# Kernel tuning notes

Hardware: AMD Instinct MI355X
Metric: run time of the kernel (lower is better)

Reference implementation:

```python
import jax, jax.numpy as jnp
import numpy as np

B, T, D = 2, 2048, 1024
H = 16
DK = D // H


def setup_inputs() -> dict:
    key = jax.random.key(0)
    ks = jax.random.split(key, 5)
    s = 1.0 / np.sqrt(D)
    return {
        "x": jax.random.normal(ks[0], (B, T, D), dtype=jnp.float32),
        "Wq": jax.random.normal(ks[1], (D, D), dtype=jnp.float32) * s,
        "bq": jnp.zeros((D,), dtype=jnp.float32),
        "Wk": jax.random.normal(ks[2], (D, D), dtype=jnp.float32) * s,
        "bk": jnp.zeros((D,), dtype=jnp.float32),
        "Wv": jax.random.normal(ks[3], (D, D), dtype=jnp.float32) * s,
        "bv": jnp.zeros((D,), dtype=jnp.float32),
        "Wo": jax.random.normal(ks[4], (D, D), dtype=jnp.float32) * s,
        "bo": jnp.zeros((D,), dtype=jnp.float32),
    }


def reference(x, Wq, bq, Wk, bk, Wv, bv, Wo, bo):
    # projections (torch Linear: x @ W.T + b; here W is stored as (in, out))
    Q = x @ Wq + bq  # (B,T,D)
    K = x @ Wk + bk
    V = x @ Wv + bv
    # split heads -> (B,H,T,dk)
    Q = Q.reshape(B, T, H, DK).transpose(0, 2, 1, 3)
    K = K.reshape(B, T, H, DK).transpose(0, 2, 1, 3)
    V = V.reshape(B, T, H, DK).transpose(0, 2, 1, 3)
    scale = 1.0 / jnp.sqrt(jnp.asarray(DK, dtype=x.dtype))
    scores = jnp.einsum("bhqd,bhkd->bhqk", Q, K) * scale  # (B,H,T,T)
    causal = jnp.tril(jnp.ones((T, T), dtype=bool))
    scores = jnp.where(causal, scores, -jnp.inf)
    weights = jax.nn.softmax(scores, axis=-1)
    # dropout is identity in eval mode
    context = jnp.einsum("bhqk,bhkd->bhqd", weights, V)
    context = context.transpose(0, 2, 1, 3).reshape(B, T, D)
    return context @ Wo + bo
```

## Files before the change

### kernel.cpp

```cpp
#include <hip/hip_runtime.h>
#include <hip/hip_bf16.h>

constexpr int Bc = 2;
constexpr int Tc = 2048;
constexpr int Mc = Bc * Tc;
constexpr float CfQ = 0.18033688011112042f;

typedef __attribute__((ext_vector_type(8))) __bf16 bf16x8;
typedef __attribute__((ext_vector_type(4))) __bf16 bf16x4;
typedef __attribute__((ext_vector_type(4))) float floatx4;

__device__ __forceinline__ void gl_lds16(const void* g, void* l) {
    __builtin_amdgcn_global_load_lds(
        (const __attribute__((address_space(1))) void*)g,
        (__attribute__((address_space(3))) void*)l, 16, 0, 0);
}

__global__ __launch_bounds__(256) void prep_all(const float* __restrict__ x,
                                                const float* __restrict__ Wq,
                                                const float* __restrict__ Wk,
                                                const float* __restrict__ Wv,
                                                const float* __restrict__ Wo,
                                                __bf16* __restrict__ xb,
                                                __bf16* __restrict__ Wqkv,
                                                __bf16* __restrict__ Wot) {
    const int z = blockIdx.z;
    const int tid = threadIdx.x;
    if (z >= 4) {
        const int lb = blockIdx.y * 16 + blockIdx.x;
        const size_t base = ((size_t)(z - 4) * 256 + lb) * 4096;
#pragma unroll
        for (int it = 0; it < 4; ++it) {
            const size_t i = base + (size_t)(it * 256 + tid) * 4;
            const float4 v = *(const float4*)(x + i);
            bf16x4 r;
            r[0] = (__bf16)v.x; r[1] = (__bf16)v.y;
            r[2] = (__bf16)v.z; r[3] = (__bf16)v.w;
            *(bf16x4*)(xb + i) = r;
        }
        return;
    }
    __shared__ float t[64][65];
    const float* W = (z == 0) ? Wq : (z == 1) ? Wk : (z == 2) ? Wv : Wo;
    __bf16* Wt = (z < 3) ? Wqkv + (size_t)z * 1024 * 1024 : Wot;
    const int k0 = blockIdx.y * 64, n0 = blockIdx.x * 64;
    const int c = tid & 63, r0 = tid >> 6;
#pragma unroll
    for (int i = 0; i < 16; ++i)
        t[r0 + i * 4][c] = W[(size_t)(k0 + r0 + i * 4) * 1024 + n0 + c];
    __syncthreads();
#pragma unroll
    for (int i = 0; i < 16; ++i) {
        const int r = r0 + i * 4;
        Wt[(size_t)(n0 + r) * 1024 + k0 + c] = (__bf16)t[c][r];
    }
}

__global__ __launch_bounds__(512, 2) void gemm_qkv(const __bf16* __restrict__ A,
                                                   const __bf16* __restrict__ Bt,
                                                   const float* __restrict__ b0,
                                                   const float* __restrict__ b1,
                                                   const float* __restrict__ b2,
                                                   __bf16* __restrict__ C,
                                                   __bf16* __restrict__ Vt) {
    constexpr int K = 1024, ldc = 2048;
    __shared__ __bf16 As[2][256 * 64];
    __shared__ __bf16 Bs[2][192 * 64];
    const int tid = threadIdx.x, lane = tid & 63, wave = tid >> 6;
    const int wm = wave >> 2, wn = wave & 3;
    const int n = blockIdx.x;
    const int xc = n & 7, ii = n >> 3;
    const int by = 2 * xc + (ii & 1), bx = ii >> 1;
    const int bm = by * 256, bn = bx * 192;
    const __bf16* Ab = A + (size_t)bm * K;
    const __bf16* Bb = Bt + (size_t)bn * K;
    const int quad = lane >> 4, tm = lane & 15;

    floatx4 acc[8][3] = {};

    auto stage = [&](int k0, int sb) {
#pragma unroll
        for (int j = 0; j < 4; ++j) {
            const int s = j * 512 + tid;
            const int row = s >> 3, lc = (s & 7) ^ (row & 7);
            gl_lds16(Ab + (size_t)row * K + k0 + lc * 8, &As[sb][s * 8]);
        }
#pragma unroll
        for (int j = 0; j < 3; ++j) {
            const int s = j * 512 + tid;
            const int row = s >> 3, lc = (s & 7) ^ (row & 7);
            gl_lds16(Bb + (size_t)row * K + k0 + lc * 8, &Bs[sb][s * 8]);
        }
    };

    stage(0, 0);

    for (int st = 0; st < 16; ++st) {
        const int buf = st & 1;
        if (st + 1 < 16) {
            stage((st + 1) * 64, buf ^ 1);
            asm volatile("s_waitcnt vmcnt(7)" ::: "memory");
        } else {
            asm volatile("s_waitcnt vmcnt(0)" ::: "memory");
        }
        __builtin_amdgcn_sched_barrier(0);
        __builtin_amdgcn_s_barrier();

        const __bf16* as = As[buf];
        const __bf16* bs = Bs[buf];
#pragma unroll
        for (int ks = 0; ks < 2; ++ks) {
            bf16x8 bfp[3], afq[8];
#pragma unroll
            for (int n2 = 0; n2 < 3; ++n2) {
                const int r = wn * 48 + n2 * 16 + tm;
                bfp[n2] = *(const bf16x8*)(
                    bs + r * 64 + (((ks * 4 + quad) ^ (r & 7)) * 8));
            }
#pragma unroll
            for (int m8 = 0; m8 < 8; ++m8) {
                const int r = wm * 128 + m8 * 16 + tm;
                afq[m8] = *(const bf16x8*)(
                    as + r * 64 + (((ks * 4 + quad) ^ (r & 7)) * 8));
            }
            __builtin_amdgcn_s_setprio(1);
#pragma unroll
            for (int m8 = 0; m8 < 8; ++m8)
#pragma unroll
                for (int n2 = 0; n2 < 3; ++n2)
                    acc[m8][n2] = __builtin_amdgcn_mfma_f32_16x16x32_bf16(
                        afq[m8], bfp[n2], acc[m8][n2], 0, 0, 0);
            __builtin_amdgcn_s_setprio(0);
        }
        __builtin_amdgcn_sched_barrier(0);
        __builtin_amdgcn_s_barrier();
    }

#pragma unroll
    for (int ni = 0; ni < 3; ++ni) {
        const int gc = bn + wn * 48 + ni * 16 + tm;
        const float bias = (gc < 1024) ? b0[gc]
                         : (gc < 2048) ? b1[gc - 1024]
                                       : b2[gc - 2048];
        const float scale = (gc < 1024) ? CfQ : 1.0f;
#pragma unroll
        for (int mi = 0; mi < 8; ++mi) {
            const int gr0 = bm + wm * 128 + mi * 16 + quad * 4;
            if (gc >= 2048) {
                bf16x4 pv;
#pragma unroll
                for (int r = 0; r < 4; ++r) pv[r] = (__bf16)(acc[mi][ni][r] + bias);
                const int bb = gr0 >> 11, tloc = gr0 & 2047;
                const int hh = (gc - 2048) >> 6, dd = gc & 63;
                const int tperm = (tloc & ~63) + ((tloc >> 2) & 3) * 16 +
                                  ((tloc >> 4) & 3) * 4;
                *(bf16x4*)(Vt + ((size_t)(bb * 16 + hh) * 64 + dd) * 2048 + tperm) = pv;
            } else {
#pragma unroll
                for (int r = 0; r < 4; ++r)
                    C[(size_t)(gr0 + r) * ldc + gc] =
                        (__bf16)((acc[mi][ni][r] + bias) * scale);
            }
        }
    }
}

__global__ __launch_bounds__(512, 2) void gemm_out(const __bf16* __restrict__ A,
                                                   const __bf16* __restrict__ Bt,
                                                   const float* __restrict__ b0,
                                                   float* __restrict__ C) {
    constexpr int K = 1024, ldc = 1024;
    __shared__ __bf16 As[2][128 * 64];
    __shared__ __bf16 Bs[2][128 * 64];
    const int tid = threadIdx.x, lane = tid & 63, wave = tid >> 6;
    const int wm = wave >> 2, wn = wave & 3;
    const int n = blockIdx.x;
    const int by = (n & 7) * 4 + ((n >> 3) & 3), bx = n >> 5;
    const int bm = by * 128, bn = bx * 128;
    const __bf16* Ab = A + (size_t)bm * K;
    const __bf16* Bb = Bt + (size_t)bn * K;
    const int quad = lane >> 4, tm = lane & 15;

    floatx4 acc[4][2] = {};

    auto stage = [&](int k0, int sb) {
#pragma unroll
        for (int j = 0; j < 2; ++j) {
            const int s = j * 512 + tid;
            const int row = s >> 3, lc = (s & 7) ^ (row & 7);
            gl_lds16(Ab + (size_t)row * K + k0 + lc * 8, &As[sb][s * 8]);
        }
#pragma unroll
        for (int j = 0; j < 2; ++j) {
            const int s = j * 512 + tid;
            const int row = s >> 3, lc = (s & 7) ^ (row & 7);
            gl_lds16(Bb + (size_t)row * K + k0 + lc * 8, &Bs[sb][s * 8]);
        }
    };

    stage(0, 0);

    for (int st = 0; st < 16; ++st) {
        const int buf = st & 1;
        if (st + 1 < 16) {
            stage((st + 1) * 64, buf ^ 1);
            asm volatile("s_waitcnt vmcnt(4)" ::: "memory");
        } else {
            asm volatile("s_waitcnt vmcnt(0)" ::: "memory");
        }
        __builtin_amdgcn_sched_barrier(0);
        __builtin_amdgcn_s_barrier();

        const __bf16* as = As[buf];
        const __bf16* bs = Bs[buf];
#pragma unroll
        for (int ks = 0; ks < 2; ++ks) {
            bf16x8 bfp[2], afq[4];
#pragma unroll
            for (int n2 = 0; n2 < 2; ++n2) {
                const int r = wn * 32 + n2 * 16 + tm;
                bfp[n2] = *(const bf16x8*)(
                    bs + r * 64 + (((ks * 4 + quad) ^ (r & 7)) * 8));
            }
#pragma unroll
            for (int m2 = 0; m2 < 4; ++m2) {
                const int r = wm * 64 + m2 * 16 + tm;
                afq[m2] = *(const bf16x8*)(
                    as + r * 64 + (((ks * 4 + quad) ^ (r & 7)) * 8));
            }
            __builtin_amdgcn_s_setprio(1);
#pragma unroll
            for (int m2 = 0; m2 < 4; ++m2)
#pragma unroll
                for (int n2 = 0; n2 < 2; ++n2)
                    acc[m2][n2] = __builtin_amdgcn_mfma_f32_16x16x32_bf16(
                        afq[m2], bfp[n2], acc[m2][n2], 0, 0, 0);
            __builtin_amdgcn_s_setprio(0);
        }
        __builtin_amdgcn_sched_barrier(0);
        __builtin_amdgcn_s_barrier();
    }

#pragma unroll
    for (int ni = 0; ni < 2; ++ni) {
        const int gc = bn + wn * 32 + ni * 16 + tm;
        const float bias = b0[gc];
#pragma unroll
        for (int mi = 0; mi < 4; ++mi) {
            const int gr0 = bm + wm * 64 + mi * 16 + quad * 4;
#pragma unroll
            for (int r = 0; r < 4; ++r)
                C[(size_t)(gr0 + r) * ldc + gc] = acc[mi][ni][r] + bias;
        }
    }
}

__global__ __launch_bounds__(512, 4) void attn_mfma(const __bf16* __restrict__ QK,
                                                    const __bf16* __restrict__ Vt,
                                                    __bf16* __restrict__ ctx) {
    constexpr float NEG = -1e30f;

    __shared__ __bf16 Ks[2][2][64 * 64];
    __shared__ __bf16 Vts[2][2][64 * 64];

    const int tid = threadIdx.x, lane = tid & 63, w = tid >> 6;
    const int g = w >> 2, wq = w & 3;
    const int c = lane & 15, quad = lane >> 4;
    const int n = blockIdx.x;
    const int bh = (n & 7) * 4 + ((n >> 3) & 3);
    const int ip = n >> 5;
    const int b = bh >> 4, h = bh & 15;

    const __bf16* Qb = QK + (size_t)(b * Tc) * 2048 + h * 64;
    const __bf16* Kb = Qb + 1024;
    const __bf16* Vtb = Vt + (size_t)bh * 64 * 2048;

    const int sw = c & 7;
    int koff0[4], koff1[4];
#pragma unroll
    for (int ni = 0; ni < 4; ++ni) {
        const int krow = ni * 16 + c;
        koff0[ni] = krow * 64 + (quad ^ sw) * 8;
        koff1[ni] = krow * 64 + ((4 + quad) ^ sw) * 8;
    }
    int voff[4][2];
#pragma unroll
    for (int di = 0; di < 4; ++di) {
        const int vrow = di * 16 + c;
#pragma unroll
        for (int pr = 0; pr < 2; ++pr)
            voff[di][pr] = vrow * 64 + ((quad * 2 + pr) ^ sw) * 8;
    }

    const int srow = tid >> 3;
    const int slc = (tid & 7) ^ (srow & 7);
    const __bf16* kgB = Kb + (size_t)srow * 2048 + slc * 8;
    const __bf16* vgB = Vtb + (size_t)srow * 2048 + slc * 8;

#pragma unroll 1
    for (int ph = 0; ph < 2; ++ph) {
        const int qt = ph ? 31 - ip : ip;
        const int nk = qt + 1;
        const int npair = (nk + 1) >> 1;

        const __bf16* qr = Qb + (size_t)(qt * 64 + wq * 16 + c) * 2048;
        const bf16x8 qf0 = *(const bf16x8*)(qr + quad * 8);
        const bf16x8 qf1 = *(const bf16x8*)(qr + 32 + quad * 8);

        floatx4 lacc = {};
        floatx4 oa[4] = {};

        auto stage = [&](int p, int sbuf) {
            const __bf16* kg = kgB + (size_t)(2 * p) * 64 * 2048;
            const __bf16* vg = vgB + 2 * p * 64;
            __bf16* kd = &Ks[sbuf][0][tid * 8];
            __bf16* vd = &Vts[sbuf][0][tid * 8];
            gl_lds16(kg, kd);
            gl_lds16(kg + (size_t)64 * 2048, kd + 4096);
            gl_lds16(vg, vd);
            gl_lds16(vg + 64, vd + 4096);
        };

        stage(0, 0);
        if (npair > 1) stage(1, 1);

        for (int kp = 0; kp < npair; ++kp) {
            const int buf = kp & 1;
            if (kp + 1 < npair) {
                asm volatile("s_waitcnt vmcnt(4)" ::: "memory");
            } else {
                asm volatile("s_waitcnt vmcnt(0)" ::: "memory");
            }
            __builtin_amdgcn_sched_barrier(0);
            __builtin_amdgcn_s_barrier();

            const int kt = 2 * kp + g;
            if (kt < nk) {
                const __bf16* ks = Ks[buf][g];
                const __bf16* vs = Vts[buf][g];

                float sv[4][4];
                __builtin_amdgcn_s_setprio(1);
#pragma unroll
                for (int ni = 0; ni < 4; ++ni) {
                    const bf16x8 kb0 = *(const bf16x8*)(ks + koff0[ni]);
                    const bf16x8 kb1 = *(const bf16x8*)(ks + koff1[ni]);
                    floatx4 a = {};
                    a = __builtin_amdgcn_mfma_f32_16x16x32_bf16(kb0, qf0, a, 0, 0, 0);
                    a = __builtin_amdgcn_mfma_f32_16x16x32_bf16(kb1, qf1, a, 0, 0, 0);
#pragma unroll
                    for (int r = 0; r < 4; ++r) sv[ni][r] = a[r];
                }
                __builtin_amdgcn_s_setprio(0);

                if (kt == qt) {
#pragma unroll
                    for (int ni = 0; ni < 4; ++ni)
#pragma unroll
                        for (int r = 0; r < 4; ++r)
                            if (ni * 16 + quad * 4 + r > wq * 16 + c) sv[ni][r] = NEG;
                }
#pragma unroll
                for (int ni = 0; ni < 4; ++ni) {
#pragma unroll
                    for (int r = 0; r < 4; ++r) sv[ni][r] = __builtin_exp2f(sv[ni][r]);
                    lacc[0] += sv[ni][0];
                    lacc[1] += sv[ni][1];
                    lacc[2] += sv[ni][2];
                    lacc[3] += sv[ni][3];
                }

                bf16x8 pb[2];
#pragma unroll
                for (int pr = 0; pr < 2; ++pr)
#pragma unroll
                    for (int j = 0; j < 4; ++j) {
                        pb[pr][j] = (__bf16)sv[pr * 2][j];
                        pb[pr][4 + j] = (__bf16)sv[pr * 2 + 1][j];
                    }

                __builtin_amdgcn_s_setprio(1);
#pragma unroll
                for (int di = 0; di < 4; ++di) {
#pragma unroll
                    for (int pr = 0; pr < 2; ++pr) {
                        const bf16x8 vf = *(const bf16x8*)(vs + voff[di][pr]);
                        oa[di] = __builtin_amdgcn_mfma_f32_16x16x32_bf16(
                            vf, pb[pr], oa[di], 0, 0, 0);
                    }
                }
                __builtin_amdgcn_s_setprio(0);
            }
            __builtin_amdgcn_sched_barrier(0);
            __builtin_amdgcn_s_barrier();
            if (kp + 2 < npair) stage(kp + 2, buf);
        }

        __syncthreads();
        float lsum = lacc[0] + lacc[1] + lacc[2] + lacc[3];
        float* sc = (float*)&Ks[0][0][0];
        if (g == 1) {
#pragma unroll
            for (int di = 0; di < 4; ++di)
                *(floatx4*)(sc + wq * 1088 + di * 256 + lane * 4) = oa[di];
            sc[wq * 1088 + 1024 + lane] = lsum;
        }
        __syncthreads();
        if (g == 0) {
#pragma unroll
            for (int di = 0; di < 4; ++di)
                oa[di] += *(const floatx4*)(sc + wq * 1088 + di * 256 + lane * 4);
            lsum += sc[wq * 1088 + 1024 + lane];
            lsum += __shfl_xor(lsum, 16);
            lsum += __shfl_xor(lsum, 32);
            const float inv = 1.f / lsum;
            __bf16* cp = ctx + (size_t)(b * Tc + qt * 64 + wq * 16 + c) * 1024 +
                         h * 64 + quad * 4;
#pragma unroll
            for (int di = 0; di < 4; ++di) {
                bf16x4 rv;
#pragma unroll
                for (int r = 0; r < 4; ++r) rv[r] = (__bf16)(oa[di][r] * inv);
                *(bf16x4*)(cp + di * 16) = rv;
            }
        }
        __syncthreads();
    }
}

extern "C" void kernel_launch(void* const* d_in, const int* in_sizes, int n_in,
                              void* d_out, int out_size, void* d_ws, size_t ws_size,
                              hipStream_t stream) {
    const float* x  = (const float*)d_in[0];
    const float* Wq = (const float*)d_in[1];
    const float* bq = (const float*)d_in[2];
    const float* Wk = (const float*)d_in[3];
    const float* bk = (const float*)d_in[4];
    const float* Wv = (const float*)d_in[5];
    const float* bv = (const float*)d_in[6];
    const float* Wo = (const float*)d_in[7];
    const float* bo = (const float*)d_in[8];

    __bf16* xb   = (__bf16*)d_ws;
    __bf16* Wqkv = xb + (size_t)Mc * 1024;
    __bf16* Wot  = Wqkv + (size_t)3072 * 1024;
    __bf16* QKb  = Wot + (size_t)1024 * 1024;
    __bf16* Vtw  = QKb + (size_t)Mc * 2048;
    __bf16* ctxb = xb;

    prep_all<<<dim3(16, 16, 8), 256, 0, stream>>>(x, Wq, Wk, Wv, Wo,
                                                  xb, Wqkv, Wot);

    gemm_qkv<<<dim3(256), 512, 0, stream>>>(xb, Wqkv, bq, bk, bv, QKb, Vtw);

    attn_mfma<<<dim3(512), 512, 0, stream>>>(QKb, Vtw, ctxb);

    gemm_out<<<dim3(256), 512, 0, stream>>>(ctxb, Wot, bo, (float*)d_out);
}
```

Baseline: 177.5 us.

## Re-tile attention warps as 2x2 query/key blocks and skip masked diagonal tile

Each warp in a group now computes a 32-query by 32-key sub-tile instead of 16 queries by 64 keys. K and V fragments loaded from LDS are reused across two query slices, which cuts LDS read traffic per MFMA. Warps whose sub-tile lies entirely above the causal diagonal skip the work. In exchange, warps in the same group now each hold partial P·V sums for the same queries, so the epilogue needs a two-stage cross-warp reduction through shared memory with extra barriers, and each warp keeps more accumulator registers.

```diff
diff --git a/kernel.cpp b/kernel.cpp
--- a/kernel.cpp
+++ b/kernel.cpp
@@ -264,7 +264,9 @@
     __shared__ __bf16 Vts[2][2][64 * 64];
 
     const int tid = threadIdx.x, lane = tid & 63, w = tid >> 6;
-    const int g = w >> 2, wq = w & 3;
+    const int g = w >> 2;
+    const int wk = w & 1;
+    const int wqh = (w >> 1) & 1;
     const int c = lane & 15, quad = lane >> 4;
     const int n = blockIdx.x;
     const int bh = (n & 7) * 4 + ((n >> 3) & 3);
@@ -276,20 +278,18 @@
     const __bf16* Vtb = Vt + (size_t)bh * 64 * 2048;
 
     const int sw = c & 7;
-    int koff0[4], koff1[4];
-#pragma unroll
-    for (int ni = 0; ni < 4; ++ni) {
-        const int krow = ni * 16 + c;
-        koff0[ni] = krow * 64 + (quad ^ sw) * 8;
-        koff1[ni] = krow * 64 + ((4 + quad) ^ sw) * 8;
-    }
-    int voff[4][2];
+    int koff0[2], koff1[2];
+#pragma unroll
+    for (int ni2 = 0; ni2 < 2; ++ni2) {
+        const int krow = (2 * wk + ni2) * 16 + c;
+        koff0[ni2] = krow * 64 + (quad ^ sw) * 8;
+        koff1[ni2] = krow * 64 + ((4 + quad) ^ sw) * 8;
+    }
+    int voff[4];
 #pragma unroll
     for (int di = 0; di < 4; ++di) {
         const int vrow = di * 16 + c;
-#pragma unroll
-        for (int pr = 0; pr < 2; ++pr)
-            voff[di][pr] = vrow * 64 + ((quad * 2 + pr) ^ sw) * 8;
+        voff[di] = vrow * 64 + ((quad * 2 + wk) ^ sw) * 8;
     }
 
     const int srow = tid >> 3;
@@ -303,12 +303,17 @@
         const int nk = qt + 1;
         const int npair = (nk + 1) >> 1;
 
-        const __bf16* qr = Qb + (size_t)(qt * 64 + wq * 16 + c) * 2048;
-        const bf16x8 qf0 = *(const bf16x8*)(qr + quad * 8);
-        const bf16x8 qf1 = *(const bf16x8*)(qr + 32 + quad * 8);
-
-        floatx4 lacc = {};
-        floatx4 oa[4] = {};
+        bf16x8 qf[2][2];
+#pragma unroll
+        for (int qs = 0; qs < 2; ++qs) {
+            const __bf16* qr =
+                Qb + (size_t)(qt * 64 + wqh * 32 + qs * 16 + c) * 2048;
+            qf[qs][0] = *(const bf16x8*)(qr + quad * 8);
+            qf[qs][1] = *(const bf16x8*)(qr + 32 + quad * 8);
+        }
+
+        floatx4 lacc[2] = {};
+        floatx4 oa[4][2] = {};
 
         auto stage = [&](int p, int sbuf) {
             const __bf16* kg = kgB + (size_t)(2 * p) * 64 * 2048;
@@ -335,61 +340,66 @@
             __builtin_amdgcn_s_barrier();
 
             const int kt = 2 * kp + g;
-            if (kt < nk) {
+            if (kt < nk && !(kt == qt && wk == 1 && wqh == 0)) {
                 const __bf16* ks = Ks[buf][g];
                 const __bf16* vs = Vts[buf][g];
 
-                float sv[4][4];
+                floatx4 sv[2][2] = {};
                 __builtin_amdgcn_s_setprio(1);
 #pragma unroll
-                for (int ni = 0; ni < 4; ++ni) {
-                    const bf16x8 kb0 = *(const bf16x8*)(ks + koff0[ni]);
-                    const bf16x8 kb1 = *(const bf16x8*)(ks + koff1[ni]);
-                    floatx4 a = {};
-                    a = __builtin_amdgcn_mfma_f32_16x16x32_bf16(kb0, qf0, a, 0, 0, 0);
-                    a = __builtin_amdgcn_mfma_f32_16x16x32_bf16(kb1, qf1, a, 0, 0, 0);
-#pragma unroll
-                    for (int r = 0; r < 4; ++r) sv[ni][r] = a[r];
-                }
-                __builtin_amdgcn_s_setprio(0);
-
-                if (kt == qt) {
-#pragma unroll
-                    for (int ni = 0; ni < 4; ++ni)
-#pragma unroll
-                        for (int r = 0; r < 4; ++r)
-                            if (ni * 16 + quad * 4 + r > wq * 16 + c) sv[ni][r] = NEG;
-                }
-#pragma unroll
-                for (int ni = 0; ni < 4; ++ni) {
-#pragma unroll
-                    for (int r = 0; r < 4; ++r) sv[ni][r] = __builtin_exp2f(sv[ni][r]);
-                    lacc[0] += sv[ni][0];
-                    lacc[1] += sv[ni][1];
-                    lacc[2] += sv[ni][2];
-                    lacc[3] += sv[ni][3];
-                }
-
-                bf16x8 pb[2];
-#pragma unroll
-                for (int pr = 0; pr < 2; ++pr)
-#pragma unroll
-                    for (int j = 0; j < 4; ++j) {
-                        pb[pr][j] = (__bf16)sv[pr * 2][j];
-                        pb[pr][4 + j] = (__bf16)sv[pr * 2 + 1][j];
-                    }
-
-                __builtin_amdgcn_s_setprio(1);
-#pragma unroll
-                for (int di = 0; di < 4; ++di) {
-#pragma unroll
-                    for (int pr = 0; pr < 2; ++pr) {
-                        const bf16x8 vf = *(const bf16x8*)(vs + voff[di][pr]);
-                        oa[di] = __builtin_amdgcn_mfma_f32_16x16x32_bf16(
-                            vf, pb[pr], oa[di], 0, 0, 0);
+                for (int ni2 = 0; ni2 < 2; ++ni2) {
+                    const bf16x8 kb0 = *(const bf16x8*)(ks + koff0[ni2]);
+                    const bf16x8 kb1 = *(const bf16x8*)(ks + koff1[ni2]);
+#pragma unroll
+                    for (int qs = 0; qs < 2; ++qs) {
+                        sv[ni2][qs] = __builtin_amdgcn_mfma_f32_16x16x32_bf16(
+                            kb0, qf[qs][0], sv[ni2][qs], 0, 0, 0);
+                        sv[ni2][qs] = __builtin_amdgcn_mfma_f32_16x16x32_bf16(
+                            kb1, qf[qs][1], sv[ni2][qs], 0, 0, 0);
                     }
                 }
                 __builtin_amdgcn_s_setprio(0);
+
+                if (kt == qt && wk == wqh) {
+#pragma unroll
+                    for (int ni2 = 0; ni2 < 2; ++ni2)
+#pragma unroll
+                        for (int qs = 0; qs < 2; ++qs)
+#pragma unroll
+                            for (int r = 0; r < 4; ++r)
+                                if (ni2 * 16 + quad * 4 + r > qs * 16 + c)
+                                    sv[ni2][qs][r] = NEG;
+                }
+#pragma unroll
+                for (int ni2 = 0; ni2 < 2; ++ni2)
+#pragma unroll
+                    for (int qs = 0; qs < 2; ++qs)
+#pragma unroll
+                        for (int r = 0; r < 4; ++r) {
+                            const float p = __builtin_exp2f(sv[ni2][qs][r]);
+                            sv[ni2][qs][r] = p;
+                            lacc[qs][r] += p;
+                        }
+
+                bf16x8 pb[2];
+#pragma unroll
+                for (int qs = 0; qs < 2; ++qs)
+#pragma unroll
+                    for (int j = 0; j < 4; ++j) {
+                        pb[qs][j] = (__bf16)sv[0][qs][j];
+                        pb[qs][4 + j] = (__bf16)sv[1][qs][j];
+                    }
+
+                __builtin_amdgcn_s_setprio(1);
+#pragma unroll
+                for (int di = 0; di < 4; ++di) {
+                    const bf16x8 vf = *(const bf16x8*)(vs + voff[di]);
+#pragma unroll
+                    for (int qs = 0; qs < 2; ++qs)
+                        oa[di][qs] = __builtin_amdgcn_mfma_f32_16x16x32_bf16(
+                            vf, pb[qs], oa[di][qs], 0, 0, 0);
+                }
+                __builtin_amdgcn_s_setprio(0);
             }
             __builtin_amdgcn_sched_barrier(0);
             __builtin_amdgcn_s_barrier();
@@ -397,31 +407,78 @@
         }
 
         __syncthreads();
-        float lsum = lacc[0] + lacc[1] + lacc[2] + lacc[3];
+        float ls0 = lacc[0][0] + lacc[0][1] + lacc[0][2] + lacc[0][3];
+        float ls1 = lacc[1][0] + lacc[1][1] + lacc[1][2] + lacc[1][3];
         float* sc = (float*)&Ks[0][0][0];
-        if (g == 1) {
+        float* scl = (float*)&Vts[0][0][0];
+        if (wk == 1) {
+            const int slot = w >> 1;
 #pragma unroll
             for (int di = 0; di < 4; ++di)
-                *(floatx4*)(sc + wq * 1088 + di * 256 + lane * 4) = oa[di];
-            sc[wq * 1088 + 1024 + lane] = lsum;
+#pragma unroll
+                for (int qs = 0; qs < 2; ++qs)
+                    *(floatx4*)(sc + slot * 2048 + (di * 2 + qs) * 256 +
+                                lane * 4) = oa[di][qs];
+            scl[slot * 128 + lane] = ls0;
+            scl[slot * 128 + 64 + lane] = ls1;
         }
         __syncthreads();
-        if (g == 0) {
+        if (wk == 0) {
+            const int slot = w >> 1;
 #pragma unroll
             for (int di = 0; di < 4; ++di)
-                oa[di] += *(const floatx4*)(sc + wq * 1088 + di * 256 + lane * 4);
-            lsum += sc[wq * 1088 + 1024 + lane];
-            lsum += __shfl_xor(lsum, 16);
-            lsum += __shfl_xor(lsum, 32);
-            const float inv = 1.f / lsum;
-            __bf16* cp = ctx + (size_t)(b * Tc + qt * 64 + wq * 16 + c) * 1024 +
-                         h * 64 + quad * 4;
-#pragma unroll
-            for (int di = 0; di < 4; ++di) {
-                bf16x4 rv;
-#pragma unroll
-                for (int r = 0; r < 4; ++r) rv[r] = (__bf16)(oa[di][r] * inv);
-                *(bf16x4*)(cp + di * 16) = rv;
+#pragma unroll
+                for (int qs = 0; qs < 2; ++qs)
+                    oa[di][qs] += *(const floatx4*)(sc + slot * 2048 +
+                                                    (di * 2 + qs) * 256 +
+                                                    lane * 4);
+            ls0 += scl[slot * 128 + lane];
+            ls1 += scl[slot * 128 + 64 + lane];
+        }
+        __syncthreads();
+        if (g == 1 && wk == 0) {
+            const int slot = (w - 4) >> 1;
+#pragma unroll
+            for (int di = 0; di < 4; ++di)
+#pragma unroll
+                for (int qs = 0; qs < 2; ++qs)
+                    *(floatx4*)(sc + slot * 2048 + (di * 2 + qs) * 256 +
+                                lane * 4) = oa[di][qs];
+            scl[slot * 128 + lane] = ls0;
+            scl[slot * 128 + 64 + lane] = ls1;
+        }
+        __syncthreads();
+        if (g == 0 && wk == 0) {
+            const int slot = w >> 1;
+#pragma unroll
+            for (int di = 0; di < 4; ++di)
+#pragma unroll
+                for (int qs = 0; qs < 2; ++qs)
+                    oa[di][qs] += *(const floatx4*)(sc + slot * 2048 +
+                                                    (di * 2 + qs) * 256 +
+                                                    lane * 4);
+            ls0 += scl[slot * 128 + lane];
+            ls1 += scl[slot * 128 + 64 + lane];
+            ls0 += __shfl_xor(ls0, 16);
+            ls0 += __shfl_xor(ls0, 32);
+            ls1 += __shfl_xor(ls1, 16);
+            ls1 += __shfl_xor(ls1, 32);
+            const float inv0 = 1.f / ls0;
+            const float inv1 = 1.f / ls1;
+#pragma unroll
+            for (int qs = 0; qs < 2; ++qs) {
+                const float inv = qs ? inv1 : inv0;
+                __bf16* cp = ctx +
+                    (size_t)(b * Tc + qt * 64 + wqh * 32 + qs * 16 + c) * 1024 +
+                    h * 64 + quad * 4;
+#pragma unroll
+                for (int di = 0; di < 4; ++di) {
+                    bf16x4 rv;
+#pragma unroll
+                    for (int r = 0; r < 4; ++r)
+                        rv[r] = (__bf16)(oa[di][qs][r] * inv);
+                    *(bf16x4*)(cp + di * 16) = rv;
+                }
             }
         }
         __syncthreads();
```

Measured after the change: 185.9 us. 1.05x slower.
